# Performance work log

Measured on AMD Instinct MI355X. Metric: run time of the kernel, lower is better.

The kernel has to match this reference:

```python
import jax, jax.numpy as jnp
import numpy as np

N_SRC, N_TGT, K, L, C_OUT = 16384, 16384, 16, 128, 2
E = N_TGT * K
MIN_VAR = 1e-3   # adf.keep_variance_fn min variance (applied in Dropout)
DROP_P = 0.2
INV_SQRT2 = np.float32(1.0 / np.sqrt(2.0))
INV_SQRT2PI = np.float32(1.0 / np.sqrt(2.0 * np.pi))


def setup_inputs() -> dict:
    key = jax.random.key(0)
    ks = jax.random.split(key, 12)
    pos_source = jax.random.uniform(ks[0], (N_SRC, 3), jnp.float32)
    pos_target = jax.random.uniform(ks[1], (N_TGT, 3), jnp.float32)
    latents = jax.random.normal(ks[2], (N_SRC, L), jnp.float32)
    var = jax.random.uniform(ks[3], (N_SRC, L), jnp.float32)
    # KNN-style edge list: each target has K source neighbors
    row = jnp.repeat(jnp.arange(N_TGT, dtype=jnp.int32), K)          # [E] target idx
    col = jax.random.randint(ks[4], (E,), 0, N_SRC, jnp.int32)       # [E] source idx
    occupancies = jax.random.randint(ks[5], (N_TGT,), 0, 2, jnp.int32)
    # fixed inverted-dropout mask (deterministic stand-in for adf.Dropout training mask)
    drop_mask = (jax.random.uniform(ks[6], (E, L)) >= DROP_P).astype(jnp.float32) / (1.0 - DROP_P)
    def init_w(k, sh):
        return jax.random.normal(k, sh, jnp.float32) * np.float32(1.0 / np.sqrt(sh[-1]))
    W_in = init_w(ks[7], (L, L + 3)); b_in = jnp.zeros((L,), jnp.float32)
    W1 = init_w(ks[8], (L, L)); b1 = jnp.zeros((L,), jnp.float32)
    W2 = init_w(ks[9], (L, L)); b2 = jnp.zeros((L,), jnp.float32)
    W_out = init_w(ks[10], (C_OUT, L)); b_out = jnp.zeros((C_OUT,), jnp.float32)
    return dict(pos_source=pos_source, pos_target=pos_target, latents=latents, var=var,
                drop_mask=drop_mask, W_in=W_in, b_in=b_in, W1=W1, b1=b1, W2=W2, b2=b2,
                W_out=W_out, b_out=b_out, row=row, col=col, occupancies=occupancies)


def _adf_linear(m, v, W, b):
    # ADF Linear: mean -> affine; variance -> through squared weights, no bias
    return m @ W.T + b, v @ (W * W).T


def _adf_relu(m, v):
    # ADF ReLU moment matching (Gast & Roth); clamp var for sqrt stability
    v = jnp.maximum(v, 1e-6)
    std = jnp.sqrt(v)
    r = m / std
    cdf = 0.5 * (1.0 + jax.lax.erf(r * INV_SQRT2))
    pdf = jnp.exp(-0.5 * r * r) * INV_SQRT2PI
    m_out = m * cdf + std * pdf
    v_out = (m * m + v) * cdf + m * std * pdf - m_out * m_out
    return m_out, v_out


def reference(pos_source, pos_target, latents, var, drop_mask, W_in, b_in, W1, b1, W2, b2, W_out, b_out, row, col, occupancies):
    pos_rel = pos_target[row] - pos_source[col]                    # [E,3]
    m = jnp.concatenate([latents[col], pos_rel], axis=1)           # [E,L+3]
    v = jnp.concatenate([var[col], pos_rel], axis=1)               # [E,L+3] (faithful: pos_rel reused as 'variance')
    m, v = _adf_linear(m, v, W_in, b_in)
    for W, b in ((W1, b1), (W2, b2)):
        m, v = _adf_relu(m, v)
        m, v = _adf_linear(m, v, W, b)
    # ADF dropout with keep_variance_fn
    m = m * drop_mask
    v = v * drop_mask * drop_mask + MIN_VAR
    m, v = _adf_linear(m, v, W_out, b_out)                         # [E,2]
    preds = m[:, 0]
    aleatoric = jnp.abs(v[:, 0]).mean()
    occ_gt = occupancies[row].astype(jnp.float32)
    # stable binary_cross_entropy_with_logits, mean reduction
    recons_loss = jnp.mean(jnp.maximum(preds, 0.0) - preds * occ_gt + jnp.log1p(jnp.exp(-jnp.abs(preds))))
    return preds, aleatoric, recons_loss, occ_gt
```

## Files before the change

kernel.cpp:

```cpp
#include <hip/hip_runtime.h>
#include <math.h>

#define E_TOT 262144
#define LDIM  128
#define XPB   272
#define MIN_VARF 0.001f
#define INV_SQRT2PIF 0.3989422804014327f
#define NBLK  (E_TOT / 64)

typedef _Float16 half8 __attribute__((ext_vector_type(8)));
typedef float    f32x4 __attribute__((ext_vector_type(4)));
typedef float    f32x2 __attribute__((ext_vector_type(2)));
typedef __attribute__((address_space(1))) const unsigned int g32;
typedef __attribute__((address_space(3))) unsigned int l32;

#define BIAS_OFF  256
#define WOUT_OFF  1792
#define BOUT_OFF  2816
#define PK_L0     4096
#define PK_L1     45056
#define PK_L2     77824
#define PART_OFF  110592

__device__ __forceinline__ short h2s(float x) {
    union U { _Float16 h; short s; } u; u.h = (_Float16)x; return u.s;
}

__device__ __forceinline__ void adf_relu(float& m, float& v) {
    float vv = fmaxf(v, 1e-6f);
    float is = __builtin_amdgcn_rsqf(vv);
    float sd = vv * is;
    float r  = m * is;
    float qq = 0.5f * r * r;
    float sp = sd * __expf(-qq) * INV_SQRT2PIF;
    const float A = 0.147f;
    float aq  = A * qq;
    float num = qq * (1.27323954f + aq);
    float den = 1.0f + aq;
    float z   = -num * __builtin_amdgcn_rcpf(den);
    float wv  = 1.0f - __expf(z);
    float s   = wv * __builtin_amdgcn_rsqf(fmaxf(wv, 1e-20f));
    float serf = copysignf(s, m);
    float cdf  = 0.5f + 0.5f * serf;
    float mo = fmaf(m, cdf, sp);
    float vo = fmaf(fmaf(m, m, vv), cdf, fmaf(m, sp, -mo * mo));
    m = mo; v = vo;
}

__global__ void prep(const float* __restrict__ W_in, const float* __restrict__ b_in,
                     const float* __restrict__ W1,   const float* __restrict__ b1,
                     const float* __restrict__ W2,   const float* __restrict__ b2,
                     const float* __restrict__ W_out,const float* __restrict__ b_out,
                     char* __restrict__ ws)
{
    int idx = blockIdx.x * 256 + threadIdx.x;
    if (idx < 6656) {
        const float* W; int Kfull; long dstoff; int entry;
        if (idx < 2560)      { entry = idx;        W = W_in; Kfull = 131; dstoff = PK_L0; }
        else if (idx < 4608) { entry = idx - 2560; W = W1;   Kfull = 128; dstoff = PK_L1; }
        else                 { entry = idx - 4608; W = W2;   Kfull = 128; dstoff = PK_L2; }
        int ks   = entry >> 9;
        int rest = entry & 511;
        int t    = rest >> 6;
        int lane = rest & 63;
        int rowi = t * 16 + (lane & 15);
        int k0   = ks * 32 + (lane >> 4) * 8;
        half8 hv;
#pragma unroll
        for (int j = 0; j < 8; ++j) {
            int k = k0 + j;
            hv[j] = (_Float16)((k < Kfull) ? W[rowi * Kfull + k] : 0.0f);
        }
        *(half8*)(ws + dstoff + (long)entry * 16) = hv;
    } else if (idx < 6656 + 384) {
        int j = idx - 6656; int layer = j >> 7; int pidx = j & 127;
        int gg = pidx >> 5, t = (pidx >> 2) & 7, r = pidx & 3;
        int n = t * 16 + gg * 4 + r;
        const float* b = layer == 0 ? b_in : (layer == 1 ? b1 : b2);
        ((float*)(ws + BIAS_OFF))[layer * 128 + pidx] = b[n];
    } else if (idx < 6656 + 384 + 256) {
        int j = idx - 6656 - 384; int path = j >> 7; int pidx = j & 127;
        int gg = pidx >> 5, t = (pidx >> 2) & 7, r = pidx & 3;
        int n = t * 16 + gg * 4 + r;
        float v = W_out[n];
        if (path) v = v * v;
        ((float*)(ws + WOUT_OFF))[path * 128 + pidx] = v;
    } else if (idx == 6656 + 384 + 256) {
        ((float*)(ws + BOUT_OFF))[0] = b_out[0];
    }
}

__global__ void __launch_bounds__(256, 2)
interp_main(const float* __restrict__ pos_source, const float* __restrict__ pos_target,
            const float* __restrict__ latents,    const float* __restrict__ varr,
            const float* __restrict__ drop_mask,
            const int* __restrict__ row, const int* __restrict__ col, const int* __restrict__ occ,
            float* __restrict__ out, char* __restrict__ ws)
{
    __shared__ __align__(16) char  Wl[40960];
    __shared__ __align__(16) short Xm[64][XPB / 2];
    __shared__ __align__(16) short Xv[64][XPB / 2];
    __shared__ __align__(16) float cbuf[648];
    __shared__ float wred[4][2];

    const int tid  = threadIdx.x;
    const int lane = tid & 63;
    const int w    = tid >> 6;
    const int q    = lane & 15;
    const int g    = lane >> 4;
    const int erow = w * 16 + q;
    const int gbase = blockIdx.x * 64;
    const int ge   = gbase + erow;
    char* xmb = (char*)&Xm[0][0];
    char* xvb = (char*)&Xv[0][0];

    {
        const char* src = ws + PK_L0;
        for (int off = w * 1024; off < 40960; off += 4096)
            __builtin_amdgcn_global_load_lds((g32*)(src + off + lane * 16), (l32*)(Wl + off), 16, 0, 0);
    }
    for (int i = tid; i < 162; i += 256)
        ((f32x4*)cbuf)[i] = ((const f32x4*)(ws + BIAS_OFF))[i];

    const int c0 = col[ge];
    const int r0 = row[ge];
    f32x4 md[8];
    {
        const f32x4* dmp = (const f32x4*)drop_mask + (size_t)ge * 32 + g;
#pragma unroll
        for (int t = 0; t < 8; ++t) md[t] = __builtin_nontemporal_load(dmp + t * 4);
    }
    const float occf = (float)occ[r0];
    const float px = pos_target[r0 * 3 + 0] - pos_source[c0 * 3 + 0];
    const float py = pos_target[r0 * 3 + 1] - pos_source[c0 * 3 + 1];
    const float pz = pos_target[r0 * 3 + 2] - pos_source[c0 * 3 + 2];

    half8 bm4[4], bv4[4];
    {
        const float* lm = latents + (long)c0 * LDIM;
        const float* lv = varr    + (long)c0 * LDIM;
#pragma unroll
        for (int ks = 0; ks < 4; ++ks) {
            const f32x4* am4 = (const f32x4*)(lm + ks * 32 + g * 8);
            const f32x4* av4 = (const f32x4*)(lv + ks * 32 + g * 8);
            f32x4 fm0 = am4[0], fm1 = am4[1];
            f32x4 fv0 = av4[0], fv1 = av4[1];
            half8 bm, bv;
#pragma unroll
            for (int j = 0; j < 4; ++j) {
                bm[j] = (_Float16)fm0[j]; bm[j + 4] = (_Float16)fm1[j];
                bv[j] = (_Float16)fv0[j]; bv[j + 4] = (_Float16)fv1[j];
            }
            bm4[ks] = bm; bv4[ks] = bv;
        }
    }

    f32x4 accm[8], accv[8];
    const f32x4 zz = {0.0f, 0.0f, 0.0f, 0.0f};
#pragma unroll
    for (int t = 0; t < 8; ++t) { accm[t] = zz; accv[t] = zz; }

    asm volatile("s_waitcnt vmcnt(0)" ::: "memory");
    __syncthreads();

    {
#pragma unroll
        for (int ks = 0; ks < 4; ++ks) {
            const char* pmk = Wl + ks * 8192 + lane * 16;
            half8 bm = bm4[ks], bv = bv4[ks];
#pragma unroll
            for (int t = 0; t < 8; ++t) {
                half8 am = *(const half8*)(pmk + t * 1024);
                half8 av = am * am;
                accm[t] = __builtin_amdgcn_mfma_f32_16x16x32_f16(am, bm, accm[t], 0, 0, 0);
                accv[t] = __builtin_amdgcn_mfma_f32_16x16x32_f16(av, bv, accv[t], 0, 0, 0);
            }
        }
        half8 bpos = {(_Float16)0.f, (_Float16)0.f, (_Float16)0.f, (_Float16)0.f,
                      (_Float16)0.f, (_Float16)0.f, (_Float16)0.f, (_Float16)0.f};
        if (g == 0) { bpos[0] = (_Float16)px; bpos[1] = (_Float16)py; bpos[2] = (_Float16)pz; }
        const char* pmk = Wl + 4 * 8192 + lane * 16;
#pragma unroll
        for (int t = 0; t < 8; ++t) {
            half8 am = *(const half8*)(pmk + t * 1024);
            half8 av = am * am;
            accm[t] = __builtin_amdgcn_mfma_f32_16x16x32_f16(am, bpos, accm[t], 0, 0, 0);
            accv[t] = __builtin_amdgcn_mfma_f32_16x16x32_f16(av, bpos, accv[t], 0, 0, 0);
        }
    }

    __syncthreads();
    {
        const char* src = ws + PK_L1;
        for (int off = w * 1024; off < 32768; off += 4096)
            __builtin_amdgcn_global_load_lds((g32*)(src + off + lane * 16), (l32*)(Wl + off), 16, 0, 0);
    }
    {
        const float* bp = cbuf + g * 32;
#pragma unroll
        for (int t = 0; t < 8; ++t) {
            float m0 = accm[t][0] + bp[t * 4 + 0], m1 = accm[t][1] + bp[t * 4 + 1];
            float m2 = accm[t][2] + bp[t * 4 + 2], m3 = accm[t][3] + bp[t * 4 + 3];
            float v0 = accv[t][0], v1 = accv[t][1], v2 = accv[t][2], v3 = accv[t][3];
            adf_relu(m0, v0); adf_relu(m1, v1); adf_relu(m2, v2); adf_relu(m3, v3);
            short4 sm; sm.x = h2s(m0); sm.y = h2s(m1); sm.z = h2s(m2); sm.w = h2s(m3);
            short4 sv; sv.x = h2s(v0); sv.y = h2s(v1); sv.z = h2s(v2); sv.w = h2s(v3);
            *(short4*)(xmb + erow * XPB + t * 32 + g * 8) = sm;
            *(short4*)(xvb + erow * XPB + t * 32 + g * 8) = sv;
        }
    }
    asm volatile("s_waitcnt vmcnt(0)" ::: "memory");
    __syncthreads();

#pragma unroll
    for (int t = 0; t < 8; ++t) { accm[t] = zz; accv[t] = zz; }
#pragma unroll
    for (int ks = 0; ks < 4; ++ks) {
        half8 bm = *(const half8*)(xmb + erow * XPB + ks * 64 + g * 16);
        half8 bv = *(const half8*)(xvb + erow * XPB + ks * 64 + g * 16);
        const char* pmk = Wl + ks * 8192 + lane * 16;
#pragma unroll
        for (int t = 0; t < 8; ++t) {
            half8 am = *(const half8*)(pmk + t * 1024);
            half8 av = am * am;
            accm[t] = __builtin_amdgcn_mfma_f32_16x16x32_f16(am, bm, accm[t], 0, 0, 0);
            accv[t] = __builtin_amdgcn_mfma_f32_16x16x32_f16(av, bv, accv[t], 0, 0, 0);
        }
    }

    __syncthreads();
    {
        const char* src = ws + PK_L2;
        for (int off = w * 1024; off < 32768; off += 4096)
            __builtin_amdgcn_global_load_lds((g32*)(src + off + lane * 16), (l32*)(Wl + off), 16, 0, 0);
    }
    {
        const float* bp = cbuf + 128 + g * 32;
#pragma unroll
        for (int t = 0; t < 8; ++t) {
            float m0 = accm[t][0] + bp[t * 4 + 0], m1 = accm[t][1] + bp[t * 4 + 1];
            float m2 = accm[t][2] + bp[t * 4 + 2], m3 = accm[t][3] + bp[t * 4 + 3];
            float v0 = accv[t][0], v1 = accv[t][1], v2 = accv[t][2], v3 = accv[t][3];
            adf_relu(m0, v0); adf_relu(m1, v1); adf_relu(m2, v2); adf_relu(m3, v3);
            short4 sm; sm.x = h2s(m0); sm.y = h2s(m1); sm.z = h2s(m2); sm.w = h2s(m3);
            short4 sv; sv.x = h2s(v0); sv.y = h2s(v1); sv.z = h2s(v2); sv.w = h2s(v3);
            *(short4*)(xmb + erow * XPB + t * 32 + g * 8) = sm;
            *(short4*)(xvb + erow * XPB + t * 32 + g * 8) = sv;
        }
    }
    asm volatile("s_waitcnt vmcnt(0)" ::: "memory");
    __syncthreads();

#pragma unroll
    for (int t = 0; t < 8; ++t) { accm[t] = zz; accv[t] = zz; }
#pragma unroll
    for (int ks = 0; ks < 4; ++ks) {
        half8 bm = *(const half8*)(xmb + erow * XPB + ks * 64 + g * 16);
        half8 bv = *(const half8*)(xvb + erow * XPB + ks * 64 + g * 16);
        const char* pmk = Wl + ks * 8192 + lane * 16;
#pragma unroll
        for (int t = 0; t < 8; ++t) {
            half8 am = *(const half8*)(pmk + t * 1024);
            half8 av = am * am;
            accm[t] = __builtin_amdgcn_mfma_f32_16x16x32_f16(am, bm, accm[t], 0, 0, 0);
            accv[t] = __builtin_amdgcn_mfma_f32_16x16x32_f16(av, bv, accv[t], 0, 0, 0);
        }
    }

    {
        float pmacc = 0.0f, pvacc = 0.0f;
        const f32x4* wmp = (const f32x4*)(cbuf + 384);
        const float* bp  = cbuf + 256 + g * 32;
#pragma unroll
        for (int t = 0; t < 8; ++t) {
            f32x4 d4 = md[t];
            f32x4 w4 = wmp[g * 8 + t];
            f32x4 s4 = wmp[32 + g * 8 + t];
            float m0 = (accm[t][0] + bp[t * 4 + 0]) * d4[0];
            float m1 = (accm[t][1] + bp[t * 4 + 1]) * d4[1];
            float m2 = (accm[t][2] + bp[t * 4 + 2]) * d4[2];
            float m3 = (accm[t][3] + bp[t * 4 + 3]) * d4[3];
            float v0 = accv[t][0] * d4[0] * d4[0] + MIN_VARF;
            float v1 = accv[t][1] * d4[1] * d4[1] + MIN_VARF;
            float v2 = accv[t][2] * d4[2] * d4[2] + MIN_VARF;
            float v3 = accv[t][3] * d4[3] * d4[3] + MIN_VARF;
            pmacc += w4[0] * m0 + w4[1] * m1 + w4[2] * m2 + w4[3] * m3;
            pvacc += s4[0] * v0 + s4[1] * v1 + s4[2] * v2 + s4[3] * v3;
        }
        pmacc += __shfl_xor(pmacc, 16, 64);
        pmacc += __shfl_xor(pmacc, 32, 64);
        pvacc += __shfl_xor(pvacc, 16, 64);
        pvacc += __shfl_xor(pvacc, 32, 64);
        float bout = cbuf[640];
        float p = pmacc + bout;
        if (lane < 16) {
            out[ge] = p;
            out[E_TOT + 2 + ge] = occf;
        }
        float a = fabsf(p);
        float loss = fmaxf(p, 0.0f) - p * occf + __logf(1.0f + __expf(-a));
        float al = fabsf(pvacc);
#pragma unroll
        for (int off = 1; off < 16; off <<= 1) {
            al   += __shfl_xor(al, off, 64);
            loss += __shfl_xor(loss, off, 64);
        }
        if (lane == 0) { wred[w][0] = al; wred[w][1] = loss; }
    }
    __syncthreads();
    if (tid == 0) {
        f32x2 s;
        s[0] = wred[0][0] + wred[1][0] + wred[2][0] + wred[3][0];
        s[1] = wred[0][1] + wred[1][1] + wred[2][1] + wred[3][1];
        *((f32x2*)(ws + PART_OFF) + blockIdx.x) = s;
    }
}

__global__ void __launch_bounds__(256)
interp_finalize(const char* __restrict__ ws, float* __restrict__ out)
{
    __shared__ float sal[4], sls[4];
    const int tid  = threadIdx.x;
    const int lane = tid & 63;
    const int w    = tid >> 6;
    float al = 0.0f, ls = 0.0f;
    const f32x2* part = (const f32x2*)(ws + PART_OFF);
    for (int i = tid; i < NBLK; i += 256) {
        f32x2 p = part[i];
        al += p[0]; ls += p[1];
    }
#pragma unroll
    for (int off = 1; off < 64; off <<= 1) {
        al += __shfl_xor(al, off, 64);
        ls += __shfl_xor(ls, off, 64);
    }
    if (lane == 0) { sal[w] = al; sls[w] = ls; }
    __syncthreads();
    if (tid == 0) {
        const float inv = 1.0f / (float)E_TOT;
        out[E_TOT]     = (sal[0] + sal[1] + sal[2] + sal[3]) * inv;
        out[E_TOT + 1] = (sls[0] + sls[1] + sls[2] + sls[3]) * inv;
    }
}

extern "C" void kernel_launch(void* const* d_in, const int* in_sizes, int n_in,
                              void* d_out, int out_size, void* d_ws, size_t ws_size,
                              hipStream_t stream) {
    (void)in_sizes; (void)n_in; (void)out_size; (void)ws_size;
    const float* pos_source = (const float*)d_in[0];
    const float* pos_target = (const float*)d_in[1];
    const float* latents    = (const float*)d_in[2];
    const float* varr       = (const float*)d_in[3];
    const float* drop_mask  = (const float*)d_in[4];
    const float* W_in       = (const float*)d_in[5];
    const float* b_in       = (const float*)d_in[6];
    const float* W1         = (const float*)d_in[7];
    const float* b1         = (const float*)d_in[8];
    const float* W2         = (const float*)d_in[9];
    const float* b2         = (const float*)d_in[10];
    const float* W_out      = (const float*)d_in[11];
    const float* b_out      = (const float*)d_in[12];
    const int*   row        = (const int*)d_in[13];
    const int*   col        = (const int*)d_in[14];
    const int*   occ        = (const int*)d_in[15];
    float* out = (float*)d_out;
    char*  ws  = (char*)d_ws;

    prep<<<29, 256, 0, stream>>>(W_in, b_in, W1, b1, W2, b2, W_out, b_out, ws);
    interp_main<<<NBLK, 256, 0, stream>>>(
        pos_source, pos_target, latents, varr, drop_mask,
        row, col, occ, out, ws);
    interp_finalize<<<1, 256, 0, stream>>>(ws, out);
}
```

Before: 153.0 us.

## Read packed weights directly from global memory instead of staging in LDS

Removes the LDS weight buffer and constant buffer, so every wave reads the packed fp16 weights and biases straight from global memory (expected to hit in L2/L1) rather than loading them into shared memory per layer. This drops several block-wide barriers and waitcnts between layers and frees about 40 KB of LDS per block, which allows raising launch bounds to 3 blocks per CU. The cost is that each wave now issues its own global loads for the weights, adding latency and cache pressure on the MFMA operand path.

```diff
diff --git a/kernel.cpp b/kernel.cpp
--- a/kernel.cpp
+++ b/kernel.cpp
@@ -11,8 +11,6 @@
 typedef _Float16 half8 __attribute__((ext_vector_type(8)));
 typedef float    f32x4 __attribute__((ext_vector_type(4)));
 typedef float    f32x2 __attribute__((ext_vector_type(2)));
-typedef __attribute__((address_space(1))) const unsigned int g32;
-typedef __attribute__((address_space(3))) unsigned int l32;
 
 #define BIAS_OFF  256
 #define WOUT_OFF  1792
@@ -90,17 +88,15 @@
     }
 }
 
-__global__ void __launch_bounds__(256, 2)
+__global__ void __launch_bounds__(256, 3)
 interp_main(const float* __restrict__ pos_source, const float* __restrict__ pos_target,
             const float* __restrict__ latents,    const float* __restrict__ varr,
             const float* __restrict__ drop_mask,
             const int* __restrict__ row, const int* __restrict__ col, const int* __restrict__ occ,
             float* __restrict__ out, char* __restrict__ ws)
 {
-    __shared__ __align__(16) char  Wl[40960];
     __shared__ __align__(16) short Xm[64][XPB / 2];
     __shared__ __align__(16) short Xv[64][XPB / 2];
-    __shared__ __align__(16) float cbuf[648];
     __shared__ float wred[4][2];
 
     const int tid  = threadIdx.x;
@@ -114,22 +110,14 @@
     char* xmb = (char*)&Xm[0][0];
     char* xvb = (char*)&Xv[0][0];
 
-    {
-        const char* src = ws + PK_L0;
-        for (int off = w * 1024; off < 40960; off += 4096)
-            __builtin_amdgcn_global_load_lds((g32*)(src + off + lane * 16), (l32*)(Wl + off), 16, 0, 0);
-    }
-    for (int i = tid; i < 162; i += 256)
-        ((f32x4*)cbuf)[i] = ((const f32x4*)(ws + BIAS_OFF))[i];
-
+    f32x4 md[8];
+    {
+        const f32x4* dmp = (const f32x4*)drop_mask + (size_t)ge * 32 + g;
+#pragma unroll
+        for (int t = 0; t < 8; ++t) md[t] = __builtin_nontemporal_load(dmp + t * 4);
+    }
     const int c0 = col[ge];
     const int r0 = row[ge];
-    f32x4 md[8];
-    {
-        const f32x4* dmp = (const f32x4*)drop_mask + (size_t)ge * 32 + g;
-#pragma unroll
-        for (int t = 0; t < 8; ++t) md[t] = __builtin_nontemporal_load(dmp + t * 4);
-    }
     const float occf = (float)occ[r0];
     const float px = pos_target[r0 * 3 + 0] - pos_source[c0 * 3 + 0];
     const float py = pos_target[r0 * 3 + 1] - pos_source[c0 * 3 + 1];
@@ -160,13 +148,11 @@
 #pragma unroll
     for (int t = 0; t < 8; ++t) { accm[t] = zz; accv[t] = zz; }
 
-    asm volatile("s_waitcnt vmcnt(0)" ::: "memory");
-    __syncthreads();
-
-    {
+    {
+        const char* pk = ws + PK_L0 + lane * 16;
 #pragma unroll
         for (int ks = 0; ks < 4; ++ks) {
-            const char* pmk = Wl + ks * 8192 + lane * 16;
+            const char* pmk = pk + ks * 8192;
             half8 bm = bm4[ks], bv = bv4[ks];
 #pragma unroll
             for (int t = 0; t < 8; ++t) {
@@ -179,7 +165,7 @@
         half8 bpos = {(_Float16)0.f, (_Float16)0.f, (_Float16)0.f, (_Float16)0.f,
                       (_Float16)0.f, (_Float16)0.f, (_Float16)0.f, (_Float16)0.f};
         if (g == 0) { bpos[0] = (_Float16)px; bpos[1] = (_Float16)py; bpos[2] = (_Float16)pz; }
-        const char* pmk = Wl + 4 * 8192 + lane * 16;
+        const char* pmk = pk + 4 * 8192;
 #pragma unroll
         for (int t = 0; t < 8; ++t) {
             half8 am = *(const half8*)(pmk + t * 1024);
@@ -187,20 +173,12 @@
             accm[t] = __builtin_amdgcn_mfma_f32_16x16x32_f16(am, bpos, accm[t], 0, 0, 0);
             accv[t] = __builtin_amdgcn_mfma_f32_16x16x32_f16(av, bpos, accv[t], 0, 0, 0);
         }
-    }
-
-    __syncthreads();
-    {
-        const char* src = ws + PK_L1;
-        for (int off = w * 1024; off < 32768; off += 4096)
-            __builtin_amdgcn_global_load_lds((g32*)(src + off + lane * 16), (l32*)(Wl + off), 16, 0, 0);
-    }
-    {
-        const float* bp = cbuf + g * 32;
+        const f32x4* bp = (const f32x4*)(ws + BIAS_OFF) + g * 8;
 #pragma unroll
         for (int t = 0; t < 8; ++t) {
-            float m0 = accm[t][0] + bp[t * 4 + 0], m1 = accm[t][1] + bp[t * 4 + 1];
-            float m2 = accm[t][2] + bp[t * 4 + 2], m3 = accm[t][3] + bp[t * 4 + 3];
+            f32x4 b4 = bp[t];
+            float m0 = accm[t][0] + b4[0], m1 = accm[t][1] + b4[1];
+            float m2 = accm[t][2] + b4[2], m3 = accm[t][3] + b4[3];
             float v0 = accv[t][0], v1 = accv[t][1], v2 = accv[t][2], v3 = accv[t][3];
             adf_relu(m0, v0); adf_relu(m1, v1); adf_relu(m2, v2); adf_relu(m3, v3);
             short4 sm; sm.x = h2s(m0); sm.y = h2s(m1); sm.z = h2s(m2); sm.w = h2s(m3);
@@ -209,37 +187,30 @@
             *(short4*)(xvb + erow * XPB + t * 32 + g * 8) = sv;
         }
     }
-    asm volatile("s_waitcnt vmcnt(0)" ::: "memory");
-    __syncthreads();
 
 #pragma unroll
     for (int t = 0; t < 8; ++t) { accm[t] = zz; accv[t] = zz; }
-#pragma unroll
-    for (int ks = 0; ks < 4; ++ks) {
-        half8 bm = *(const half8*)(xmb + erow * XPB + ks * 64 + g * 16);
-        half8 bv = *(const half8*)(xvb + erow * XPB + ks * 64 + g * 16);
-        const char* pmk = Wl + ks * 8192 + lane * 16;
+    {
+        const char* pk = ws + PK_L1 + lane * 16;
+#pragma unroll
+        for (int ks = 0; ks < 4; ++ks) {
+            half8 bm = *(const half8*)(xmb + erow * XPB + ks * 64 + g * 16);
+            half8 bv = *(const half8*)(xvb + erow * XPB + ks * 64 + g * 16);
+            const char* pmk = pk + ks * 8192;
+#pragma unroll
+            for (int t = 0; t < 8; ++t) {
+                half8 am = *(const half8*)(pmk + t * 1024);
+                half8 av = am * am;
+                accm[t] = __builtin_amdgcn_mfma_f32_16x16x32_f16(am, bm, accm[t], 0, 0, 0);
+                accv[t] = __builtin_amdgcn_mfma_f32_16x16x32_f16(av, bv, accv[t], 0, 0, 0);
+            }
+        }
+        const f32x4* bp = (const f32x4*)(ws + BIAS_OFF) + 32 + g * 8;
 #pragma unroll
         for (int t = 0; t < 8; ++t) {
-            half8 am = *(const half8*)(pmk + t * 1024);
-            half8 av = am * am;
-            accm[t] = __builtin_amdgcn_mfma_f32_16x16x32_f16(am, bm, accm[t], 0, 0, 0);
-            accv[t] = __builtin_amdgcn_mfma_f32_16x16x32_f16(av, bv, accv[t], 0, 0, 0);
-        }
-    }
-
-    __syncthreads();
-    {
-        const char* src = ws + PK_L2;
-        for (int off = w * 1024; off < 32768; off += 4096)
-            __builtin_amdgcn_global_load_lds((g32*)(src + off + lane * 16), (l32*)(Wl + off), 16, 0, 0);
-    }
-    {
-        const float* bp = cbuf + 128 + g * 32;
-#pragma unroll
-        for (int t = 0; t < 8; ++t) {
-            float m0 = accm[t][0] + bp[t * 4 + 0], m1 = accm[t][1] + bp[t * 4 + 1];
-            float m2 = accm[t][2] + bp[t * 4 + 2], m3 = accm[t][3] + bp[t * 4 + 3];
+            f32x4 b4 = bp[t];
+            float m0 = accm[t][0] + b4[0], m1 = accm[t][1] + b4[1];
+            float m2 = accm[t][2] + b4[2], m3 = accm[t][3] + b4[3];
             float v0 = accv[t][0], v1 = accv[t][1], v2 = accv[t][2], v3 = accv[t][3];
             adf_relu(m0, v0); adf_relu(m1, v1); adf_relu(m2, v2); adf_relu(m3, v3);
             short4 sm; sm.x = h2s(m0); sm.y = h2s(m1); sm.z = h2s(m2); sm.w = h2s(m3);
@@ -248,38 +219,40 @@
             *(short4*)(xvb + erow * XPB + t * 32 + g * 8) = sv;
         }
     }
-    asm volatile("s_waitcnt vmcnt(0)" ::: "memory");
-    __syncthreads();
 
 #pragma unroll
     for (int t = 0; t < 8; ++t) { accm[t] = zz; accv[t] = zz; }
-#pragma unroll
-    for (int ks = 0; ks < 4; ++ks) {
-        half8 bm = *(const half8*)(xmb + erow * XPB + ks * 64 + g * 16);
-        half8 bv = *(const half8*)(xvb + erow * XPB + ks * 64 + g * 16);
-        const char* pmk = Wl + ks * 8192 + lane * 16;
+    {
+        const char* pk = ws + PK_L2 + lane * 16;
+#pragma unroll
+        for (int ks = 0; ks < 4; ++ks) {
+            half8 bm = *(const half8*)(xmb + erow * XPB + ks * 64 + g * 16);
+            half8 bv = *(const half8*)(xvb + erow * XPB + ks * 64 + g * 16);
+            const char* pmk = pk + ks * 8192;
+#pragma unroll
+            for (int t = 0; t < 8; ++t) {
+                half8 am = *(const half8*)(pmk + t * 1024);
+                half8 av = am * am;
+                accm[t] = __builtin_amdgcn_mfma_f32_16x16x32_f16(am, bm, accm[t], 0, 0, 0);
+                accv[t] = __builtin_amdgcn_mfma_f32_16x16x32_f16(av, bv, accv[t], 0, 0, 0);
+            }
+        }
+    }
+
+    {
+        float pmacc = 0.0f, pvacc = 0.0f;
+        const f32x4* wmp = (const f32x4*)(ws + WOUT_OFF);
+        const f32x4* bp  = (const f32x4*)(ws + BIAS_OFF) + 64 + g * 8;
 #pragma unroll
         for (int t = 0; t < 8; ++t) {
-            half8 am = *(const half8*)(pmk + t * 1024);
-            half8 av = am * am;
-            accm[t] = __builtin_amdgcn_mfma_f32_16x16x32_f16(am, bm, accm[t], 0, 0, 0);
-            accv[t] = __builtin_amdgcn_mfma_f32_16x16x32_f16(av, bv, accv[t], 0, 0, 0);
-        }
-    }
-
-    {
-        float pmacc = 0.0f, pvacc = 0.0f;
-        const f32x4* wmp = (const f32x4*)(cbuf + 384);
-        const float* bp  = cbuf + 256 + g * 32;
-#pragma unroll
-        for (int t = 0; t < 8; ++t) {
+            f32x4 b4 = bp[t];
             f32x4 d4 = md[t];
             f32x4 w4 = wmp[g * 8 + t];
             f32x4 s4 = wmp[32 + g * 8 + t];
-            float m0 = (accm[t][0] + bp[t * 4 + 0]) * d4[0];
-            float m1 = (accm[t][1] + bp[t * 4 + 1]) * d4[1];
-            float m2 = (accm[t][2] + bp[t * 4 + 2]) * d4[2];
-            float m3 = (accm[t][3] + bp[t * 4 + 3]) * d4[3];
+            float m0 = (accm[t][0] + b4[0]) * d4[0];
+            float m1 = (accm[t][1] + b4[1]) * d4[1];
+            float m2 = (accm[t][2] + b4[2]) * d4[2];
+            float m3 = (accm[t][3] + b4[3]) * d4[3];
             float v0 = accv[t][0] * d4[0] * d4[0] + MIN_VARF;
             float v1 = accv[t][1] * d4[1] * d4[1] + MIN_VARF;
             float v2 = accv[t][2] * d4[2] * d4[2] + MIN_VARF;
@@ -291,7 +264,7 @@
         pmacc += __shfl_xor(pmacc, 32, 64);
         pvacc += __shfl_xor(pvacc, 16, 64);
         pvacc += __shfl_xor(pvacc, 32, 64);
-        float bout = cbuf[640];
+        float bout = *(const float*)(ws + BOUT_OFF);
         float p = pmacc + bout;
         if (lane < 16) {
             out[ge] = p;
```

Measured after the change: 156.5 us. +2.3%, slower.
